# Optimization experiments

Measured on AMD Instinct MI355X. Metric: run time of the kernel, lower is better.

The kernel has to match this reference:

```python
import jax, jax.numpy as jnp
import numpy as np

B, C, H, W = 16, 512, 32, 32
GROUPS = 8
EPS = 1e-5


def setup_inputs() -> dict:
    key = jax.random.key(0)
    ks = jax.random.split(key, 7)
    s = 1.0 / np.sqrt(C)
    return {
        "x": jax.random.normal(ks[0], (B, C, H, W), dtype=jnp.float32),
        "gamma": jnp.ones((C,), dtype=jnp.float32),
        "beta": jnp.zeros((C,), dtype=jnp.float32),
        "w_qkv": jax.random.normal(ks[1], (3 * C, C), dtype=jnp.float32) * s,
        "b_qkv": jnp.zeros((3 * C,), dtype=jnp.float32),
        "w_proj": jax.random.normal(ks[2], (C, C), dtype=jnp.float32) * s,
        "b_proj": jnp.zeros((C,), dtype=jnp.float32),
    }


def group_norm(x, gamma, beta):
    b, c, h, w = x.shape
    xg = x.reshape(b, GROUPS, c // GROUPS, h, w)
    mean = xg.mean(axis=(2, 3, 4), keepdims=True)
    var = xg.var(axis=(2, 3, 4), keepdims=True)
    xn = ((xg - mean) * jax.lax.rsqrt(var + EPS)).reshape(b, c, h, w)
    return xn * gamma[None, :, None, None] + beta[None, :, None, None]


def reference(x, gamma, beta, w_qkv, b_qkv, w_proj, b_proj):
    b, c, h, w = x.shape
    n = h * w
    hn = group_norm(x, gamma, beta)
    # 1x1 conv == channel matmul: [3C, C] x [B, C, N] -> [B, 3C, N]
    qkv = jnp.einsum('oc,bcn->bon', w_qkv, hn.reshape(b, c, n)) + b_qkv[None, :, None]
    q, k, v = jnp.split(qkv, 3, axis=1)  # each [B, C, N]
    scale = c ** (-0.5)
    # scores [B, N, N]: q^T k
    attn = jax.nn.softmax(jnp.einsum('bcn,bcm->bnm', q, k) * scale, axis=-1)
    out = jnp.einsum('bnm,bcm->bcn', attn, v)  # [B, C, N]
    proj = jnp.einsum('oc,bcn->bon', w_proj, out) + b_proj[None, :, None]
    return x + proj.reshape(b, c, h, w)
```

## Files before the change

kernel.cpp:

```cpp
#include <hip/hip_runtime.h>


#define BATCH 16
#define CCH 512
#define NSP 1024
#define EPSV 1e-5f
#define BK 32
#define HT 4096

typedef short bf16x8 __attribute__((ext_vector_type(8)));
typedef float f32x4 __attribute__((ext_vector_type(4)));

__device__ __forceinline__ unsigned short f2bf(float f) {
    unsigned int u = __float_as_uint(f);
    u += 0x7FFF + ((u >> 16) & 1);
    return (unsigned short)(u >> 16);
}

__device__ __forceinline__ void glds16(const void* g, void* l) {
    __builtin_amdgcn_global_load_lds(
        (const __attribute__((address_space(1))) unsigned int*)g,
        (__attribute__((address_space(3))) unsigned int*)l, 16, 0, 0);
}

#define MEMF asm volatile("" ::: "memory")
#define VMW(n) asm volatile("s_waitcnt vmcnt(" #n ")" ::: "memory")

#define XCD_MAP(GX_LOG2, PER, xv, yv, bv)                 \
    const int lin_ = blockIdx.x;                          \
    const int xcd_ = lin_ & 7;                            \
    int slot_ = lin_ >> 3;                                \
    const int hi_ = (slot_ >= (PER)) ? 1 : 0;             \
    const int bv = xcd_ + 8 * hi_;                        \
    slot_ -= hi_ * (PER);                                 \
    const int xv = slot_ & ((1 << (GX_LOG2)) - 1);        \
    const int yv = slot_ >> (GX_LOG2);

__device__ __forceinline__ void gemm128_dbuf(
    const unsigned short* __restrict__ Ag, const unsigned short* __restrict__ Bg,
    int astr, int bstr, int ktot, short* L, f32x4* acc) {
    const int t = threadIdx.x;
    const int w = t >> 6, lane = t & 63;
    const int wr = (w >> 1) * 64, wc = (w & 1) * 64;
    const int fr = lane & 15;
    const int fsw = (((lane >> 4) ^ (fr & 3)) * 8);
    const int r0 = t >> 2;
    const int kc = (((t & 3) ^ (r0 & 3)) * 8);
    const unsigned short* Ap0 = Ag + (size_t)r0 * astr + kc;
    const unsigned short* Ap1 = Ag + (size_t)(r0 + 64) * astr + kc;
    const unsigned short* Bp0 = Bg + (size_t)r0 * bstr + kc;
    const unsigned short* Bp1 = Bg + (size_t)(r0 + 64) * bstr + kc;
    short* lw = L + w * 512;

#define STG(bf, kk) do {                                  \
    short* aw_ = lw + (bf) * (4 * HT);                    \
    short* bw_ = aw_ + 2 * HT;                            \
    glds16(Ap0 + (kk), aw_);                              \
    glds16(Ap1 + (kk), aw_ + 2048);                       \
    glds16(Ap0 + (kk) + 32, aw_ + HT);                    \
    glds16(Ap1 + (kk) + 32, aw_ + HT + 2048);             \
    glds16(Bp0 + (kk), bw_);                              \
    glds16(Bp1 + (kk), bw_ + 2048);                       \
    glds16(Bp0 + (kk) + 32, bw_ + HT);                    \
    glds16(Bp1 + (kk) + 32, bw_ + HT + 2048);             \
  } while (0)

#define CMP(bf) do {                                                        \
    _Pragma("unroll")                                                       \
    for (int h = 0; h < 2; h++) {                                           \
        const short* Ab_ = L + (bf) * (4 * HT) + h * HT;                    \
        const short* Bb_ = Ab_ + 2 * HT;                                    \
        bf16x8 af[4], bfr[4];                                               \
        _Pragma("unroll")                                                   \
        for (int mi = 0; mi < 4; mi++)                                      \
            af[mi] = *(const bf16x8*)(Ab_ + (wr + mi * 16 + fr) * BK + fsw);\
        _Pragma("unroll")                                                   \
        for (int ni = 0; ni < 4; ni++)                                      \
            bfr[ni] = *(const bf16x8*)(Bb_ + (wc + ni * 16 + fr) * BK + fsw);\
        _Pragma("unroll")                                                   \
        for (int mi = 0; mi < 4; mi++)                                      \
            _Pragma("unroll")                                               \
            for (int ni = 0; ni < 4; ni++)                                  \
                acc[mi * 4 + ni] = __builtin_amdgcn_mfma_f32_16x16x32_bf16( \
                    af[mi], bfr[ni], acc[mi * 4 + ni], 0, 0, 0);            \
    } } while (0)

    STG(0, 0);
    for (int k0 = 0; k0 < ktot; k0 += 128) {
        STG(1, k0 + 64);
        VMW(8);
        MEMF; __builtin_amdgcn_s_barrier();
        CMP(0);
        MEMF; __builtin_amdgcn_s_barrier();
        const int kb = (k0 + 128 < ktot) ? k0 + 128 : 0;
        STG(0, kb);
        VMW(8);
        MEMF; __builtin_amdgcn_s_barrier();
        CMP(1);
        MEMF; __builtin_amdgcn_s_barrier();
    }
    VMW(0);
#undef STG
#undef CMP
}

__device__ __forceinline__ void gemm128_sb(
    const unsigned short* __restrict__ Ag, const unsigned short* __restrict__ Bg,
    int astr, int bstr, int ktot, short* Al, short* Bl, f32x4* acc) {
    const int t = threadIdx.x;
    const int w = t >> 6, lane = t & 63;
    const int wr = (w >> 1) * 64, wc = (w & 1) * 64;
    const int fr = lane & 15;
    const int fsw = (((lane >> 4) ^ (fr & 3)) * 8);
    const int r0 = t >> 2;
    const int kc = (((t & 3) ^ (r0 & 3)) * 8);
    const unsigned short* Ap0 = Ag + (size_t)r0 * astr + kc;
    const unsigned short* Ap1 = Ag + (size_t)(r0 + 64) * astr + kc;
    const unsigned short* Bp0 = Bg + (size_t)r0 * bstr + kc;
    const unsigned short* Bp1 = Bg + (size_t)(r0 + 64) * bstr + kc;
    short* Alw = Al + w * 512;
    short* Blw = Bl + w * 512;
    for (int k0 = 0; k0 < ktot; k0 += 64) {
        glds16(Ap0 + k0, Alw);
        glds16(Ap1 + k0, Alw + 2048);
        glds16(Ap0 + k0 + 32, Alw + HT);
        glds16(Ap1 + k0 + 32, Alw + HT + 2048);
        glds16(Bp0 + k0, Blw);
        glds16(Bp1 + k0, Blw + 2048);
        glds16(Bp0 + k0 + 32, Blw + HT);
        glds16(Bp1 + k0 + 32, Blw + HT + 2048);
        __syncthreads();
#pragma unroll
        for (int h = 0; h < 2; h++) {
            const short* Ab = Al + h * HT;
            const short* Bb = Bl + h * HT;
            bf16x8 af[4], bfr[4];
#pragma unroll
            for (int mi = 0; mi < 4; mi++)
                af[mi] = *(const bf16x8*)(Ab + (wr + mi * 16 + fr) * BK + fsw);
#pragma unroll
            for (int ni = 0; ni < 4; ni++)
                bfr[ni] = *(const bf16x8*)(Bb + (wc + ni * 16 + fr) * BK + fsw);
#pragma unroll
            for (int mi = 0; mi < 4; mi++)
#pragma unroll
                for (int ni = 0; ni < 4; ni++)
                    acc[mi * 4 + ni] = __builtin_amdgcn_mfma_f32_16x16x32_bf16(
                        af[mi], bfr[ni], acc[mi * 4 + ni], 0, 0, 0);
        }
        __syncthreads();
    }
}

#define EPI_SETUP()                                          \
    const int t = threadIdx.x, lane = t & 63, w = t >> 6;    \
    const int wr = (w >> 1) * 64, wc = (w & 1) * 64;         \
    const int fr = lane & 15, rr0 = (lane >> 4) * 4;

#define ACC_INIT(acc)                                        \
    f32x4 acc[16];                                           \
    _Pragma("unroll") for (int i = 0; i < 16; i++)           \
        acc[i] = (f32x4){0.f, 0.f, 0.f, 0.f};

__global__ __launch_bounds__(256) void setup_k(
    const float* __restrict__ x, float* __restrict__ stats,
    const float* __restrict__ wa, unsigned short* __restrict__ oa, int na4,
    const float* __restrict__ wb, unsigned short* __restrict__ ob, int nb4,
    float* __restrict__ Lsum, const float* __restrict__ bqv,
    unsigned short* __restrict__ wv_t, float* __restrict__ puv) {
    const int t = threadIdx.x;
    const int bx = blockIdx.x;
    __shared__ float rs[4], rq[4];
    __shared__ __align__(16) unsigned short Tt[64 * 72];
    if (bx < 128) {
        const int bg = bx;
        const float4* xp = (const float4*)(x + (size_t)bg * 65536);
        float s = 0.f, q = 0.f;
#pragma unroll
        for (int i = 0; i < 64; i++) {
            float4 v = xp[t + i * 256];
            s += v.x + v.y + v.z + v.w;
            q += v.x * v.x + v.y * v.y + v.z * v.z + v.w * v.w;
        }
#pragma unroll
        for (int off = 32; off; off >>= 1) {
            s += __shfl_down(s, off);
            q += __shfl_down(q, off);
        }
        const int wave = t >> 6, lane = t & 63;
        if (lane == 0) { rs[wave] = s; rq[wave] = q; }
        __syncthreads();
        if (t == 0) {
            float S = rs[0] + rs[1] + rs[2] + rs[3];
            float Q = rq[0] + rq[1] + rq[2] + rq[3];
            const float inv = 1.f / 65536.f;
            float mean = S * inv;
            float var = Q * inv - mean * mean;
            stats[bg * 2] = mean;
            stats[bg * 2 + 1] = rsqrtf(var + EPSV);
        }
    } else if (bx < 896) {
        int i = (bx - 128) * 256 + t;
        const float* src;
        unsigned short* dst;
        int j;
        if (i < na4) { src = wa; dst = oa; j = i; }
        else { j = i - na4; if (j >= nb4) return; src = wb; dst = ob; }
        float4 v = ((const float4*)src)[j];
        ushort4 o;
        o.x = f2bf(v.x); o.y = f2bf(v.y); o.z = f2bf(v.z); o.w = f2bf(v.w);
        ((ushort4*)dst)[j] = o;
    } else if (bx < 912) {
        int i = (bx - 896) * 256 + t;
        ((float4*)Lsum)[i] = (float4){0.f, 0.f, 0.f, 0.f};
    } else if (bx < 976) {
        const int r = bx - 912;
        const float* src = wa + (size_t)2 * 512 * 512;
        const int to = (r >> 3) * 64, tc = (r & 7) * 64;
        const int ol = t >> 2, cs = t & 3;
#pragma unroll
        for (int j = 0; j < 4; j++) {
            float4 v = *(const float4*)(src + (size_t)(to + ol) * 512 + tc + cs * 16 + j * 4);
            int c = cs * 16 + j * 4;
            Tt[(c + 0) * 72 + ol] = f2bf(v.x);
            Tt[(c + 1) * 72 + ol] = f2bf(v.y);
            Tt[(c + 2) * 72 + ol] = f2bf(v.z);
            Tt[(c + 3) * 72 + ol] = f2bf(v.w);
        }
        __syncthreads();
        const int cl = t >> 2, os = t & 3;
        unsigned short* d = wv_t + (size_t)(tc + cl) * 512 + to + os * 16;
        const unsigned short* s2 = Tt + cl * 72 + os * 16;
        *(uint4*)d = *(const uint4*)s2;
        *(uint4*)(d + 8) = *(const uint4*)(s2 + 8);
    } else {
        const int o = (bx - 976) * 256 + t;
        const float* wr_ = wb + (size_t)o * 512;
        const float* bv = bqv + 1024;
        float s = 0.f;
        for (int vv = 0; vv < 512; vv += 4) {
            s += wr_[vv] * bv[vv] + wr_[vv + 1] * bv[vv + 1]
               + wr_[vv + 2] * bv[vv + 2] + wr_[vv + 3] * bv[vv + 3];
        }
        puv[o] = s;
    }
}

__global__ __launch_bounds__(256) void gn_tr_k(
    const float* __restrict__ x, const float* __restrict__ gamma,
    const float* __restrict__ beta, const float* __restrict__ stats,
    unsigned short* __restrict__ hn_t,
    const unsigned short* __restrict__ wp_bf, const unsigned short* __restrict__ wv_t,
    unsigned short* __restrict__ wpv_bf) {
    __shared__ __align__(16) short SM[4 * HT];
    const int lin = blockIdx.x;
    const int t = threadIdx.x;
    if (lin < 16) {
        const int ot = (lin >> 2) * 128, ct2 = (lin & 3) * 128;
        ACC_INIT(acc);
        gemm128_sb(wp_bf + (size_t)ot * 512, wv_t + (size_t)ct2 * 512,
                   512, 512, 512, SM, SM + 2 * HT, acc);
        EPI_SETUP();
#pragma unroll
        for (int ni = 0; ni < 4; ni++) {
            int col = ct2 + wc + ni * 16 + fr;
#pragma unroll
            for (int mi = 0; mi < 4; mi++) {
                int row = ot + wr + mi * 16 + rr0;
#pragma unroll
                for (int r = 0; r < 4; r++)
                    wpv_bf[(size_t)(row + r) * 512 + col] = f2bf(acc[mi * 4 + ni][r]);
            }
        }
        return;
    }
    const int l2 = lin - 16;
    const int nt = l2 & 15, ct = (l2 >> 4) & 7, b = l2 >> 7;
    unsigned short* T = (unsigned short*)SM;
    const float mean = stats[(b * 8 + ct) * 2];
    const float rstd = stats[(b * 8 + ct) * 2 + 1];
    const int cl = t >> 2, nc = t & 3;
    const int c = ct * 64 + cl;
    const float ga = gamma[c] * rstd;
    const float be = beta[c] - mean * ga;
    const float4* xp = (const float4*)(x + ((size_t)b * CCH + c) * NSP + nt * 64);
#pragma unroll
    for (int j = 0; j < 4; j++) {
        float4 v = xp[nc * 4 + j];
        int n = nc * 16 + j * 4;
        T[(n + 0) * 72 + cl] = f2bf(v.x * ga + be);
        T[(n + 1) * 72 + cl] = f2bf(v.y * ga + be);
        T[(n + 2) * 72 + cl] = f2bf(v.z * ga + be);
        T[(n + 3) * 72 + cl] = f2bf(v.w * ga + be);
    }
    __syncthreads();
    const int nl = t >> 2, cc = t & 3;
    unsigned short* dst = hn_t + ((size_t)b * NSP + nt * 64 + nl) * CCH + ct * 64 + cc * 16;
    const unsigned short* src = T + nl * 72 + cc * 16;
    *(uint4*)dst = *(const uint4*)src;
    *(uint4*)(dst + 8) = *(const uint4*)(src + 8);
}

__global__ __launch_bounds__(256) void gemm_qku_k(
    const unsigned short* __restrict__ hn_t, const unsigned short* __restrict__ wq,
    const float* __restrict__ bq, const unsigned short* __restrict__ wpv_bf,
    const float* __restrict__ puv, unsigned short* __restrict__ QKt,
    unsigned short* __restrict__ Ub) {
    __shared__ __align__(16) short L[8 * HT];
    XCD_MAP(3, 96, xb, y, b);
    const int ntc = xb * 128;
    ACC_INIT(acc);
    if (y < 8) {
        const int mt = y * 128;
        gemm128_dbuf(hn_t + ((size_t)b * NSP + mt) * CCH,
                     wq + (size_t)ntc * CCH, CCH, CCH, CCH, L, acc);
        unsigned short* Ob = QKt + (size_t)b * NSP * 1024;
        EPI_SETUP();
#pragma unroll
        for (int ni = 0; ni < 4; ni++) {
            int col = ntc + wc + ni * 16 + fr;
            float bias = bq[col];
#pragma unroll
            for (int mi = 0; mi < 4; mi++) {
                int row = mt + wr + mi * 16 + rr0;
#pragma unroll
                for (int r = 0; r < 4; r++)
                    Ob[(size_t)(row + r) * 1024 + col] = f2bf(acc[mi * 4 + ni][r] + bias);
            }
        }
    } else {
        const int mt = (y - 8) * 128;
        gemm128_dbuf(wpv_bf + (size_t)mt * 512,
                     hn_t + ((size_t)b * NSP + ntc) * CCH, 512, CCH, 512, L, acc);
        unsigned short* Ob = Ub + (size_t)b * CCH * NSP;
        EPI_SETUP();
#pragma unroll
        for (int mi = 0; mi < 4; mi++) {
            int row = mt + wr + mi * 16 + rr0;
#pragma unroll
            for (int r = 0; r < 4; r++) {
                float bias = puv[row + r];
#pragma unroll
                for (int ni = 0; ni < 4; ni++) {
                    int col = ntc + wc + ni * 16 + fr;
                    Ob[(size_t)(row + r) * NSP + col] = f2bf(acc[mi * 4 + ni][r] + bias);
                }
            }
        }
    }
}

__global__ __launch_bounds__(256) void gemm_scores_k(
    const unsigned short* __restrict__ QKt, unsigned short* __restrict__ expS,
    float* __restrict__ Lsum) {
    __shared__ __align__(16) short L[8 * HT];
    XCD_MAP(3, 64, xb, yb, b);
    const int nt = xb * 128, mt = yb * 128;
    const unsigned short* base = QKt + (size_t)b * NSP * 1024;
    ACC_INIT(acc);
    gemm128_dbuf(base + (size_t)mt * 1024, base + (size_t)nt * 1024 + 512,
                 1024, 1024, 512, L, acc);
    unsigned short* Ob = expS + (size_t)b * NSP * NSP;
    float* Ls = Lsum + (size_t)b * NSP;
    const float scale = 0.044194173824159216f;
    EPI_SETUP();
#pragma unroll
    for (int mi = 0; mi < 4; mi++) {
#pragma unroll
        for (int r = 0; r < 4; r++) {
            const int row = mt + wr + mi * 16 + rr0 + r;
            float rs = 0.f;
#pragma unroll
            for (int ni = 0; ni < 4; ni++) {
                int col = nt + wc + ni * 16 + fr;
                float e = __expf(acc[mi * 4 + ni][r] * scale);
                Ob[(size_t)row * NSP + col] = f2bf(e);
                rs += e;
            }
            rs += __shfl_xor(rs, 1);
            rs += __shfl_xor(rs, 2);
            rs += __shfl_xor(rs, 4);
            rs += __shfl_xor(rs, 8);
            if (fr == 0) atomicAdd(&Ls[row], rs);
        }
    }
}

__global__ __launch_bounds__(256) void gemm_pu_k(
    const unsigned short* __restrict__ Ub, const unsigned short* __restrict__ expS,
    const float* __restrict__ Lsum, const float* __restrict__ x,
    const float* __restrict__ bp, float* __restrict__ out) {
    __shared__ __align__(16) short L[8 * HT];
    XCD_MAP(3, 32, xb, yb, b);
    const int nt = xb * 128, ot = yb * 128;
    ACC_INIT(acc);
    gemm128_dbuf(Ub + ((size_t)b * CCH + ot) * NSP,
                 expS + ((size_t)b * NSP + nt) * NSP, NSP, NSP, NSP, L, acc);
    const float* Ls = Lsum + (size_t)b * NSP;
    const size_t bbase = (size_t)b * CCH * NSP;
    EPI_SETUP();
#pragma unroll
    for (int ni = 0; ni < 4; ni++) {
        int col = nt + wc + ni * 16 + fr;
        float invl = __builtin_amdgcn_rcpf(Ls[col]);
#pragma unroll
        for (int mi = 0; mi < 4; mi++) {
            int row = ot + wr + mi * 16 + rr0;
#pragma unroll
            for (int r = 0; r < 4; r++) {
                size_t idx = bbase + (size_t)(row + r) * NSP + col;
                out[idx] = x[idx] + bp[row + r] + acc[mi * 4 + ni][r] * invl;
            }
        }
    }
}

extern "C" void kernel_launch(void* const* d_in, const int* in_sizes, int n_in,
                              void* d_out, int out_size, void* d_ws, size_t ws_size,
                              hipStream_t stream) {
    const float* x = (const float*)d_in[0];
    const float* gamma = (const float*)d_in[1];
    const float* beta = (const float*)d_in[2];
    const float* w_qkv = (const float*)d_in[3];
    const float* b_qkv = (const float*)d_in[4];
    const float* w_proj = (const float*)d_in[5];
    const float* b_proj = (const float*)d_in[6];
    float* out = (float*)d_out;

    char* ws = (char*)d_ws;
    const size_t MB = 1048576;
    const size_t KB = 1024;
    unsigned short* wqkv_bf = (unsigned short*)ws;
    unsigned short* wproj_bf = (unsigned short*)(ws + 1572864);
    float* stats = (float*)(ws + 2 * MB);
    float* Lsum = (float*)(ws + 2 * MB + 64 * KB);
    float* puv = (float*)(ws + 2 * MB + 128 * KB);
    unsigned short* wv_t = (unsigned short*)(ws + 2 * MB + 256 * KB);
    unsigned short* wpv_bf = (unsigned short*)(ws + 3 * MB);
    unsigned short* hn_t = (unsigned short*)(ws + 4 * MB);
    unsigned short* QKt = (unsigned short*)(ws + 24 * MB);
    unsigned short* Ub = (unsigned short*)(ws + 60 * MB);
    unsigned short* expS = (unsigned short*)(ws + 80 * MB);

    setup_k<<<978, 256, 0, stream>>>(x, stats, w_qkv, wqkv_bf, 131072,
                                     w_proj, wproj_bf, 65536, Lsum, b_qkv,
                                     wv_t, puv);
    gn_tr_k<<<2064, 256, 0, stream>>>(x, gamma, beta, stats, hn_t,
                                      wproj_bf, wv_t, wpv_bf);
    gemm_qku_k<<<1536, 256, 0, stream>>>(hn_t, wqkv_bf, b_qkv, wpv_bf, puv,
                                         QKt, Ub);
    gemm_scores_k<<<1024, 256, 0, stream>>>(QKt, expS, Lsum);
    gemm_pu_k<<<512, 256, 0, stream>>>(Ub, expS, Lsum, x, b_proj, out);
}
```

Measured before the change: 204.6 us.

## Split group-norm statistics over more blocks and revert GEMMs to single-buffered loop

```diff
diff --git a/kernel.cpp b/kernel.cpp
--- a/kernel.cpp
+++ b/kernel.cpp
@@ -36,75 +36,7 @@
     const int xv = slot_ & ((1 << (GX_LOG2)) - 1);        \
     const int yv = slot_ >> (GX_LOG2);
 
-__device__ __forceinline__ void gemm128_dbuf(
-    const unsigned short* __restrict__ Ag, const unsigned short* __restrict__ Bg,
-    int astr, int bstr, int ktot, short* L, f32x4* acc) {
-    const int t = threadIdx.x;
-    const int w = t >> 6, lane = t & 63;
-    const int wr = (w >> 1) * 64, wc = (w & 1) * 64;
-    const int fr = lane & 15;
-    const int fsw = (((lane >> 4) ^ (fr & 3)) * 8);
-    const int r0 = t >> 2;
-    const int kc = (((t & 3) ^ (r0 & 3)) * 8);
-    const unsigned short* Ap0 = Ag + (size_t)r0 * astr + kc;
-    const unsigned short* Ap1 = Ag + (size_t)(r0 + 64) * astr + kc;
-    const unsigned short* Bp0 = Bg + (size_t)r0 * bstr + kc;
-    const unsigned short* Bp1 = Bg + (size_t)(r0 + 64) * bstr + kc;
-    short* lw = L + w * 512;
-
-#define STG(bf, kk) do {                                  \
-    short* aw_ = lw + (bf) * (4 * HT);                    \
-    short* bw_ = aw_ + 2 * HT;                            \
-    glds16(Ap0 + (kk), aw_);                              \
-    glds16(Ap1 + (kk), aw_ + 2048);                       \
-    glds16(Ap0 + (kk) + 32, aw_ + HT);                    \
-    glds16(Ap1 + (kk) + 32, aw_ + HT + 2048);             \
-    glds16(Bp0 + (kk), bw_);                              \
-    glds16(Bp1 + (kk), bw_ + 2048);                       \
-    glds16(Bp0 + (kk) + 32, bw_ + HT);                    \
-    glds16(Bp1 + (kk) + 32, bw_ + HT + 2048);             \
-  } while (0)
-
-#define CMP(bf) do {                                                        \
-    _Pragma("unroll")                                                       \
-    for (int h = 0; h < 2; h++) {                                           \
-        const short* Ab_ = L + (bf) * (4 * HT) + h * HT;                    \
-        const short* Bb_ = Ab_ + 2 * HT;                                    \
-        bf16x8 af[4], bfr[4];                                               \
-        _Pragma("unroll")                                                   \
-        for (int mi = 0; mi < 4; mi++)                                      \
-            af[mi] = *(const bf16x8*)(Ab_ + (wr + mi * 16 + fr) * BK + fsw);\
-        _Pragma("unroll")                                                   \
-        for (int ni = 0; ni < 4; ni++)                                      \
-            bfr[ni] = *(const bf16x8*)(Bb_ + (wc + ni * 16 + fr) * BK + fsw);\
-        _Pragma("unroll")                                                   \
-        for (int mi = 0; mi < 4; mi++)                                      \
-            _Pragma("unroll")                                               \
-            for (int ni = 0; ni < 4; ni++)                                  \
-                acc[mi * 4 + ni] = __builtin_amdgcn_mfma_f32_16x16x32_bf16( \
-                    af[mi], bfr[ni], acc[mi * 4 + ni], 0, 0, 0);            \
-    } } while (0)
-
-    STG(0, 0);
-    for (int k0 = 0; k0 < ktot; k0 += 128) {
-        STG(1, k0 + 64);
-        VMW(8);
-        MEMF; __builtin_amdgcn_s_barrier();
-        CMP(0);
-        MEMF; __builtin_amdgcn_s_barrier();
-        const int kb = (k0 + 128 < ktot) ? k0 + 128 : 0;
-        STG(0, kb);
-        VMW(8);
-        MEMF; __builtin_amdgcn_s_barrier();
-        CMP(1);
-        MEMF; __builtin_amdgcn_s_barrier();
-    }
-    VMW(0);
-#undef STG
-#undef CMP
-}
-
-__device__ __forceinline__ void gemm128_sb(
+__device__ __forceinline__ void gemm128_loop(
     const unsigned short* __restrict__ Ag, const unsigned short* __restrict__ Bg,
     int astr, int bstr, int ktot, short* Al, short* Bl, f32x4* acc) {
     const int t = threadIdx.x;
@@ -152,6 +84,74 @@
     }
 }
 
+__device__ __forceinline__ void gemm128_dbuf(
+    const unsigned short* __restrict__ Ag, const unsigned short* __restrict__ Bg,
+    int astr, int bstr, int ktot, short* L, f32x4* acc) {
+    const int t = threadIdx.x;
+    const int w = t >> 6, lane = t & 63;
+    const int wr = (w >> 1) * 64, wc = (w & 1) * 64;
+    const int fr = lane & 15;
+    const int fsw = (((lane >> 4) ^ (fr & 3)) * 8);
+    const int r0 = t >> 2;
+    const int kc = (((t & 3) ^ (r0 & 3)) * 8);
+    const unsigned short* Ap0 = Ag + (size_t)r0 * astr + kc;
+    const unsigned short* Ap1 = Ag + (size_t)(r0 + 64) * astr + kc;
+    const unsigned short* Bp0 = Bg + (size_t)r0 * bstr + kc;
+    const unsigned short* Bp1 = Bg + (size_t)(r0 + 64) * bstr + kc;
+    short* lw = L + w * 512;
+
+#define STG(bf, kk) do {                                  \
+    short* aw_ = lw + (bf) * (4 * HT);                    \
+    short* bw_ = aw_ + 2 * HT;                            \
+    glds16(Ap0 + (kk), aw_);                              \
+    glds16(Ap1 + (kk), aw_ + 2048);                       \
+    glds16(Ap0 + (kk) + 32, aw_ + HT);                    \
+    glds16(Ap1 + (kk) + 32, aw_ + HT + 2048);             \
+    glds16(Bp0 + (kk), bw_);                              \
+    glds16(Bp1 + (kk), bw_ + 2048);                       \
+    glds16(Bp0 + (kk) + 32, bw_ + HT);                    \
+    glds16(Bp1 + (kk) + 32, bw_ + HT + 2048);             \
+  } while (0)
+
+#define CMP(bf) do {                                                        \
+    _Pragma("unroll")                                                       \
+    for (int h = 0; h < 2; h++) {                                           \
+        const short* Ab_ = L + (bf) * (4 * HT) + h * HT;                    \
+        const short* Bb_ = Ab_ + 2 * HT;                                    \
+        bf16x8 af[4], bfr[4];                                               \
+        _Pragma("unroll")                                                   \
+        for (int mi = 0; mi < 4; mi++)                                      \
+            af[mi] = *(const bf16x8*)(Ab_ + (wr + mi * 16 + fr) * BK + fsw);\
+        _Pragma("unroll")                                                   \
+        for (int ni = 0; ni < 4; ni++)                                      \
+            bfr[ni] = *(const bf16x8*)(Bb_ + (wc + ni * 16 + fr) * BK + fsw);\
+        _Pragma("unroll")                                                   \
+        for (int mi = 0; mi < 4; mi++)                                      \
+            _Pragma("unroll")                                               \
+            for (int ni = 0; ni < 4; ni++)                                  \
+                acc[mi * 4 + ni] = __builtin_amdgcn_mfma_f32_16x16x32_bf16( \
+                    af[mi], bfr[ni], acc[mi * 4 + ni], 0, 0, 0);            \
+    } } while (0)
+
+    STG(0, 0);
+    for (int k0 = 0; k0 < ktot; k0 += 128) {
+        STG(1, k0 + 64);
+        VMW(8);
+        MEMF; __builtin_amdgcn_s_barrier();
+        CMP(0);
+        MEMF; __builtin_amdgcn_s_barrier();
+        const int kb = (k0 + 128 < ktot) ? k0 + 128 : 0;
+        STG(0, kb);
+        VMW(8);
+        MEMF; __builtin_amdgcn_s_barrier();
+        CMP(1);
+        MEMF; __builtin_amdgcn_s_barrier();
+    }
+    VMW(0);
+#undef STG
+#undef CMP
+}
+
 #define EPI_SETUP()                                          \
     const int t = threadIdx.x, lane = t & 63, w = t >> 6;    \
     const int wr = (w >> 1) * 64, wc = (w & 1) * 64;         \
@@ -163,7 +163,7 @@
         acc[i] = (f32x4){0.f, 0.f, 0.f, 0.f};
 
 __global__ __launch_bounds__(256) void setup_k(
-    const float* __restrict__ x, float* __restrict__ stats,
+    const float* __restrict__ x, float* __restrict__ sp,
     const float* __restrict__ wa, unsigned short* __restrict__ oa, int na4,
     const float* __restrict__ wb, unsigned short* __restrict__ ob, int nb4,
     float* __restrict__ Lsum, const float* __restrict__ bqv,
@@ -172,35 +172,30 @@
     const int bx = blockIdx.x;
     __shared__ float rs[4], rq[4];
     __shared__ __align__(16) unsigned short Tt[64 * 72];
-    if (bx < 128) {
-        const int bg = bx;
-        const float4* xp = (const float4*)(x + (size_t)bg * 65536);
-        float s = 0.f, q = 0.f;
-#pragma unroll
-        for (int i = 0; i < 64; i++) {
+    if (bx < 512) {
+        const int bg = bx >> 2, q = bx & 3;
+        const float4* xp = (const float4*)(x + (size_t)bg * 65536 + q * 16384);
+        float s = 0.f, qq = 0.f;
+#pragma unroll
+        for (int i = 0; i < 16; i++) {
             float4 v = xp[t + i * 256];
             s += v.x + v.y + v.z + v.w;
-            q += v.x * v.x + v.y * v.y + v.z * v.z + v.w * v.w;
+            qq += v.x * v.x + v.y * v.y + v.z * v.z + v.w * v.w;
         }
 #pragma unroll
         for (int off = 32; off; off >>= 1) {
             s += __shfl_down(s, off);
-            q += __shfl_down(q, off);
+            qq += __shfl_down(qq, off);
         }
         const int wave = t >> 6, lane = t & 63;
-        if (lane == 0) { rs[wave] = s; rq[wave] = q; }
+        if (lane == 0) { rs[wave] = s; rq[wave] = qq; }
         __syncthreads();
         if (t == 0) {
-            float S = rs[0] + rs[1] + rs[2] + rs[3];
-            float Q = rq[0] + rq[1] + rq[2] + rq[3];
-            const float inv = 1.f / 65536.f;
-            float mean = S * inv;
-            float var = Q * inv - mean * mean;
-            stats[bg * 2] = mean;
-            stats[bg * 2 + 1] = rsqrtf(var + EPSV);
-        }
-    } else if (bx < 896) {
-        int i = (bx - 128) * 256 + t;
+            sp[bx * 2] = rs[0] + rs[1] + rs[2] + rs[3];
+            sp[bx * 2 + 1] = rq[0] + rq[1] + rq[2] + rq[3];
+        }
+    } else if (bx < 1280) {
+        int i = (bx - 512) * 256 + t;
         const float* src;
         unsigned short* dst;
         int j;
@@ -210,11 +205,11 @@
         ushort4 o;
         o.x = f2bf(v.x); o.y = f2bf(v.y); o.z = f2bf(v.z); o.w = f2bf(v.w);
         ((ushort4*)dst)[j] = o;
-    } else if (bx < 912) {
-        int i = (bx - 896) * 256 + t;
+    } else if (bx < 1296) {
+        int i = (bx - 1280) * 256 + t;
         ((float4*)Lsum)[i] = (float4){0.f, 0.f, 0.f, 0.f};
-    } else if (bx < 976) {
-        const int r = bx - 912;
+    } else if (bx < 1360) {
+        const int r = bx - 1296;
         const float* src = wa + (size_t)2 * 512 * 512;
         const int to = (r >> 3) * 64, tc = (r & 7) * 64;
         const int ol = t >> 2, cs = t & 3;
@@ -234,7 +229,7 @@
         *(uint4*)d = *(const uint4*)s2;
         *(uint4*)(d + 8) = *(const uint4*)(s2 + 8);
     } else {
-        const int o = (bx - 976) * 256 + t;
+        const int o = (bx - 1360) * 256 + t;
         const float* wr_ = wb + (size_t)o * 512;
         const float* bv = bqv + 1024;
         float s = 0.f;
@@ -248,7 +243,7 @@
 
 __global__ __launch_bounds__(256) void gn_tr_k(
     const float* __restrict__ x, const float* __restrict__ gamma,
-    const float* __restrict__ beta, const float* __restrict__ stats,
+    const float* __restrict__ beta, const float* __restrict__ sp,
     unsigned short* __restrict__ hn_t,
     const unsigned short* __restrict__ wp_bf, const unsigned short* __restrict__ wv_t,
     unsigned short* __restrict__ wpv_bf) {
@@ -258,8 +253,8 @@
     if (lin < 16) {
         const int ot = (lin >> 2) * 128, ct2 = (lin & 3) * 128;
         ACC_INIT(acc);
-        gemm128_sb(wp_bf + (size_t)ot * 512, wv_t + (size_t)ct2 * 512,
-                   512, 512, 512, SM, SM + 2 * HT, acc);
+        gemm128_loop(wp_bf + (size_t)ot * 512, wv_t + (size_t)ct2 * 512,
+                     512, 512, 512, SM, SM + 2 * HT, acc);
         EPI_SETUP();
 #pragma unroll
         for (int ni = 0; ni < 4; ni++) {
@@ -277,8 +272,16 @@
     const int l2 = lin - 16;
     const int nt = l2 & 15, ct = (l2 >> 4) & 7, b = l2 >> 7;
     unsigned short* T = (unsigned short*)SM;
-    const float mean = stats[(b * 8 + ct) * 2];
-    const float rstd = stats[(b * 8 + ct) * 2 + 1];
+    const int bg = b * 8 + ct;
+    float S = 0.f, Q = 0.f;
+#pragma unroll
+    for (int qq = 0; qq < 4; qq++) {
+        S += sp[(bg * 4 + qq) * 2];
+        Q += sp[(bg * 4 + qq) * 2 + 1];
+    }
+    const float inv = 1.f / 65536.f;
+    const float mean = S * inv;
+    const float rstd = rsqrtf(Q * inv - mean * mean + EPSV);
     const int cl = t >> 2, nc = t & 3;
     const int c = ct * 64 + cl;
     const float ga = gamma[c] * rstd;
@@ -306,14 +309,14 @@
     const float* __restrict__ bq, const unsigned short* __restrict__ wpv_bf,
     const float* __restrict__ puv, unsigned short* __restrict__ QKt,
     unsigned short* __restrict__ Ub) {
-    __shared__ __align__(16) short L[8 * HT];
+    __shared__ __align__(16) short Al[2 * HT], Bl[2 * HT];
     XCD_MAP(3, 96, xb, y, b);
     const int ntc = xb * 128;
     ACC_INIT(acc);
     if (y < 8) {
         const int mt = y * 128;
-        gemm128_dbuf(hn_t + ((size_t)b * NSP + mt) * CCH,
-                     wq + (size_t)ntc * CCH, CCH, CCH, CCH, L, acc);
+        gemm128_loop(hn_t + ((size_t)b * NSP + mt) * CCH,
+                     wq + (size_t)ntc * CCH, CCH, CCH, CCH, Al, Bl, acc);
         unsigned short* Ob = QKt + (size_t)b * NSP * 1024;
         EPI_SETUP();
 #pragma unroll
@@ -330,8 +333,8 @@
         }
     } else {
         const int mt = (y - 8) * 128;
-        gemm128_dbuf(wpv_bf + (size_t)mt * 512,
-                     hn_t + ((size_t)b * NSP + ntc) * CCH, 512, CCH, 512, L, acc);
+        gemm128_loop(wpv_bf + (size_t)mt * 512,
+                     hn_t + ((size_t)b * NSP + ntc) * CCH, 512, CCH, 512, Al, Bl, acc);
         unsigned short* Ob = Ub + (size_t)b * CCH * NSP;
         EPI_SETUP();
 #pragma unroll
@@ -353,13 +356,13 @@
 __global__ __launch_bounds__(256) void gemm_scores_k(
     const unsigned short* __restrict__ QKt, unsigned short* __restrict__ expS,
     float* __restrict__ Lsum) {
-    __shared__ __align__(16) short L[8 * HT];
+    __shared__ __align__(16) short Al[2 * HT], Bl[2 * HT];
     XCD_MAP(3, 64, xb, yb, b);
     const int nt = xb * 128, mt = yb * 128;
     const unsigned short* base = QKt + (size_t)b * NSP * 1024;
     ACC_INIT(acc);
-    gemm128_dbuf(base + (size_t)mt * 1024, base + (size_t)nt * 1024 + 512,
-                 1024, 1024, 512, L, acc);
+    gemm128_loop(base + (size_t)mt * 1024, base + (size_t)nt * 1024 + 512,
+                 1024, 1024, 512, Al, Bl, acc);
     unsigned short* Ob = expS + (size_t)b * NSP * NSP;
     float* Ls = Lsum + (size_t)b * NSP;
     const float scale = 0.044194173824159216f;
@@ -432,7 +435,7 @@
     const size_t KB = 1024;
     unsigned short* wqkv_bf = (unsigned short*)ws;
     unsigned short* wproj_bf = (unsigned short*)(ws + 1572864);
-    float* stats = (float*)(ws + 2 * MB);
+    float* sp = (float*)(ws + 2 * MB);
     float* Lsum = (float*)(ws + 2 * MB + 64 * KB);
     float* puv = (float*)(ws + 2 * MB + 128 * KB);
     unsigned short* wv_t = (unsigned short*)(ws + 2 * MB + 256 * KB);
@@ -442,10 +445,10 @@
     unsigned short* Ub = (unsigned short*)(ws + 60 * MB);
     unsigned short* expS = (unsigned short*)(ws + 80 * MB);
 
-    setup_k<<<978, 256, 0, stream>>>(x, stats, w_qkv, wqkv_bf, 131072,
-                                     w_proj, wproj_bf, 65536, Lsum, b_qkv,
-                                     wv_t, puv);
-    gn_tr_k<<<2064, 256, 0, stream>>>(x, gamma, beta, stats, hn_t,
+    setup_k<<<1362, 256, 0, stream>>>(x, sp, w_qkv, wqkv_bf, 131072,
+                                      w_proj, wproj_bf, 65536, Lsum, b_qkv,
+                                      wv_t, puv);
+    gn_tr_k<<<2064, 256, 0, stream>>>(x, gamma, beta, sp, hn_t,
                                       wproj_bf, wv_t, wpv_bf);
     gemm_qku_k<<<1536, 256, 0, stream>>>(hn_t, wqkv_bf, b_qkv, wpv_bf, puv,
                                          QKt, Ub);
```

Result: slower. 212.1 us (+3.7%).

## Use 8-wave 512-thread blocks for the 128x128 bf16 GEMM kernels

Applied to the files above, without the earlier changes.

```diff
diff --git a/kernel.cpp b/kernel.cpp
--- a/kernel.cpp
+++ b/kernel.cpp
@@ -36,65 +36,58 @@
     const int xv = slot_ & ((1 << (GX_LOG2)) - 1);        \
     const int yv = slot_ >> (GX_LOG2);
 
-__device__ __forceinline__ void gemm128_dbuf(
+__device__ __forceinline__ void gemm128_dbuf8(
     const unsigned short* __restrict__ Ag, const unsigned short* __restrict__ Bg,
     int astr, int bstr, int ktot, short* L, f32x4* acc) {
     const int t = threadIdx.x;
     const int w = t >> 6, lane = t & 63;
-    const int wr = (w >> 1) * 64, wc = (w & 1) * 64;
+    const int wr = (w >> 2) * 64, wc = (w & 3) * 32;
     const int fr = lane & 15;
     const int fsw = (((lane >> 4) ^ (fr & 3)) * 8);
     const int r0 = t >> 2;
     const int kc = (((t & 3) ^ (r0 & 3)) * 8);
     const unsigned short* Ap0 = Ag + (size_t)r0 * astr + kc;
-    const unsigned short* Ap1 = Ag + (size_t)(r0 + 64) * astr + kc;
     const unsigned short* Bp0 = Bg + (size_t)r0 * bstr + kc;
-    const unsigned short* Bp1 = Bg + (size_t)(r0 + 64) * bstr + kc;
     short* lw = L + w * 512;
 
 #define STG(bf, kk) do {                                  \
-    short* aw_ = lw + (bf) * (4 * HT);                    \
-    short* bw_ = aw_ + 2 * HT;                            \
-    glds16(Ap0 + (kk), aw_);                              \
-    glds16(Ap1 + (kk), aw_ + 2048);                       \
-    glds16(Ap0 + (kk) + 32, aw_ + HT);                    \
-    glds16(Ap1 + (kk) + 32, aw_ + HT + 2048);             \
-    glds16(Bp0 + (kk), bw_);                              \
-    glds16(Bp1 + (kk), bw_ + 2048);                       \
-    glds16(Bp0 + (kk) + 32, bw_ + HT);                    \
-    glds16(Bp1 + (kk) + 32, bw_ + HT + 2048);             \
+    short* p_ = lw + (bf) * (4 * HT);                     \
+    glds16(Ap0 + (kk), p_);                               \
+    glds16(Ap0 + (kk) + 32, p_ + HT);                     \
+    glds16(Bp0 + (kk), p_ + 2 * HT);                      \
+    glds16(Bp0 + (kk) + 32, p_ + 3 * HT);                 \
   } while (0)
 
 #define CMP(bf) do {                                                        \
     _Pragma("unroll")                                                       \
     for (int h = 0; h < 2; h++) {                                           \
         const short* Ab_ = L + (bf) * (4 * HT) + h * HT;                    \
-        const short* Bb_ = Ab_ + 2 * HT;                                    \
-        bf16x8 af[4], bfr[4];                                               \
+        const short* Bb_ = L + (bf) * (4 * HT) + (2 + h) * HT;              \
+        bf16x8 af[4], bfr[2];                                               \
         _Pragma("unroll")                                                   \
         for (int mi = 0; mi < 4; mi++)                                      \
             af[mi] = *(const bf16x8*)(Ab_ + (wr + mi * 16 + fr) * BK + fsw);\
         _Pragma("unroll")                                                   \
-        for (int ni = 0; ni < 4; ni++)                                      \
+        for (int ni = 0; ni < 2; ni++)                                      \
             bfr[ni] = *(const bf16x8*)(Bb_ + (wc + ni * 16 + fr) * BK + fsw);\
         _Pragma("unroll")                                                   \
         for (int mi = 0; mi < 4; mi++)                                      \
             _Pragma("unroll")                                               \
-            for (int ni = 0; ni < 4; ni++)                                  \
-                acc[mi * 4 + ni] = __builtin_amdgcn_mfma_f32_16x16x32_bf16( \
-                    af[mi], bfr[ni], acc[mi * 4 + ni], 0, 0, 0);            \
+            for (int ni = 0; ni < 2; ni++)                                  \
+                acc[mi * 2 + ni] = __builtin_amdgcn_mfma_f32_16x16x32_bf16( \
+                    af[mi], bfr[ni], acc[mi * 2 + ni], 0, 0, 0);            \
     } } while (0)
 
     STG(0, 0);
     for (int k0 = 0; k0 < ktot; k0 += 128) {
         STG(1, k0 + 64);
-        VMW(8);
+        VMW(4);
         MEMF; __builtin_amdgcn_s_barrier();
         CMP(0);
         MEMF; __builtin_amdgcn_s_barrier();
         const int kb = (k0 + 128 < ktot) ? k0 + 128 : 0;
         STG(0, kb);
-        VMW(8);
+        VMW(4);
         MEMF; __builtin_amdgcn_s_barrier();
         CMP(1);
         MEMF; __builtin_amdgcn_s_barrier();
@@ -157,9 +150,19 @@
     const int wr = (w >> 1) * 64, wc = (w & 1) * 64;         \
     const int fr = lane & 15, rr0 = (lane >> 4) * 4;
 
+#define EPI8()                                               \
+    const int t = threadIdx.x, lane = t & 63, w8 = t >> 6;   \
+    const int wr = (w8 >> 2) * 64, wc = (w8 & 3) * 32;       \
+    const int fr = lane & 15, rr0 = (lane >> 4) * 4;
+
 #define ACC_INIT(acc)                                        \
     f32x4 acc[16];                                           \
     _Pragma("unroll") for (int i = 0; i < 16; i++)           \
+        acc[i] = (f32x4){0.f, 0.f, 0.f, 0.f};
+
+#define ACC_INIT8(acc)                                       \
+    f32x4 acc[8];                                            \
+    _Pragma("unroll") for (int i = 0; i < 8; i++)            \
         acc[i] = (f32x4){0.f, 0.f, 0.f, 0.f};
 
 __global__ __launch_bounds__(256) void setup_k(
@@ -301,7 +304,7 @@
     *(uint4*)(dst + 8) = *(const uint4*)(src + 8);
 }
 
-__global__ __launch_bounds__(256) void gemm_qku_k(
+__global__ __launch_bounds__(512) void gemm_qku_k(
     const unsigned short* __restrict__ hn_t, const unsigned short* __restrict__ wq,
     const float* __restrict__ bq, const unsigned short* __restrict__ wpv_bf,
     const float* __restrict__ puv, unsigned short* __restrict__ QKt,
@@ -309,15 +312,15 @@
     __shared__ __align__(16) short L[8 * HT];
     XCD_MAP(3, 96, xb, y, b);
     const int ntc = xb * 128;
-    ACC_INIT(acc);
+    ACC_INIT8(acc);
     if (y < 8) {
         const int mt = y * 128;
-        gemm128_dbuf(hn_t + ((size_t)b * NSP + mt) * CCH,
-                     wq + (size_t)ntc * CCH, CCH, CCH, CCH, L, acc);
+        gemm128_dbuf8(hn_t + ((size_t)b * NSP + mt) * CCH,
+                      wq + (size_t)ntc * CCH, CCH, CCH, CCH, L, acc);
         unsigned short* Ob = QKt + (size_t)b * NSP * 1024;
-        EPI_SETUP();
-#pragma unroll
-        for (int ni = 0; ni < 4; ni++) {
+        EPI8();
+#pragma unroll
+        for (int ni = 0; ni < 2; ni++) {
             int col = ntc + wc + ni * 16 + fr;
             float bias = bq[col];
 #pragma unroll
@@ -325,15 +328,15 @@
                 int row = mt + wr + mi * 16 + rr0;
 #pragma unroll
                 for (int r = 0; r < 4; r++)
-                    Ob[(size_t)(row + r) * 1024 + col] = f2bf(acc[mi * 4 + ni][r] + bias);
+                    Ob[(size_t)(row + r) * 1024 + col] = f2bf(acc[mi * 2 + ni][r] + bias);
             }
         }
     } else {
         const int mt = (y - 8) * 128;
-        gemm128_dbuf(wpv_bf + (size_t)mt * 512,
-                     hn_t + ((size_t)b * NSP + ntc) * CCH, 512, CCH, 512, L, acc);
+        gemm128_dbuf8(wpv_bf + (size_t)mt * 512,
+                      hn_t + ((size_t)b * NSP + ntc) * CCH, 512, CCH, 512, L, acc);
         unsigned short* Ob = Ub + (size_t)b * CCH * NSP;
-        EPI_SETUP();
+        EPI8();
 #pragma unroll
         for (int mi = 0; mi < 4; mi++) {
             int row = mt + wr + mi * 16 + rr0;
@@ -341,29 +344,29 @@
             for (int r = 0; r < 4; r++) {
                 float bias = puv[row + r];
 #pragma unroll
-                for (int ni = 0; ni < 4; ni++) {
+                for (int ni = 0; ni < 2; ni++) {
                     int col = ntc + wc + ni * 16 + fr;
-                    Ob[(size_t)(row + r) * NSP + col] = f2bf(acc[mi * 4 + ni][r] + bias);
+                    Ob[(size_t)(row + r) * NSP + col] = f2bf(acc[mi * 2 + ni][r] + bias);
                 }
             }
         }
     }
 }
 
-__global__ __launch_bounds__(256) void gemm_scores_k(
+__global__ __launch_bounds__(512) void gemm_scores_k(
     const unsigned short* __restrict__ QKt, unsigned short* __restrict__ expS,
     float* __restrict__ Lsum) {
     __shared__ __align__(16) short L[8 * HT];
     XCD_MAP(3, 64, xb, yb, b);
     const int nt = xb * 128, mt = yb * 128;
     const unsigned short* base = QKt + (size_t)b * NSP * 1024;
-    ACC_INIT(acc);
-    gemm128_dbuf(base + (size_t)mt * 1024, base + (size_t)nt * 1024 + 512,
-                 1024, 1024, 512, L, acc);
+    ACC_INIT8(acc);
+    gemm128_dbuf8(base + (size_t)mt * 1024, base + (size_t)nt * 1024 + 512,
+                  1024, 1024, 512, L, acc);
     unsigned short* Ob = expS + (size_t)b * NSP * NSP;
     float* Ls = Lsum + (size_t)b * NSP;
     const float scale = 0.044194173824159216f;
-    EPI_SETUP();
+    EPI8();
 #pragma unroll
     for (int mi = 0; mi < 4; mi++) {
 #pragma unroll
@@ -371,9 +374,9 @@
             const int row = mt + wr + mi * 16 + rr0 + r;
             float rs = 0.f;
 #pragma unroll
-            for (int ni = 0; ni < 4; ni++) {
+            for (int ni = 0; ni < 2; ni++) {
                 int col = nt + wc + ni * 16 + fr;
-                float e = __expf(acc[mi * 4 + ni][r] * scale);
+                float e = __expf(acc[mi * 2 + ni][r] * scale);
                 Ob[(size_t)row * NSP + col] = f2bf(e);
                 rs += e;
             }
@@ -386,21 +389,21 @@
     }
 }
 
-__global__ __launch_bounds__(256) void gemm_pu_k(
+__global__ __launch_bounds__(512) void gemm_pu_k(
     const unsigned short* __restrict__ Ub, const unsigned short* __restrict__ expS,
     const float* __restrict__ Lsum, const float* __restrict__ x,
     const float* __restrict__ bp, float* __restrict__ out) {
     __shared__ __align__(16) short L[8 * HT];
     XCD_MAP(3, 32, xb, yb, b);
     const int nt = xb * 128, ot = yb * 128;
-    ACC_INIT(acc);
-    gemm128_dbuf(Ub + ((size_t)b * CCH + ot) * NSP,
-                 expS + ((size_t)b * NSP + nt) * NSP, NSP, NSP, NSP, L, acc);
+    ACC_INIT8(acc);
+    gemm128_dbuf8(Ub + ((size_t)b * CCH + ot) * NSP,
+                  expS + ((size_t)b * NSP + nt) * NSP, NSP, NSP, NSP, L, acc);
     const float* Ls = Lsum + (size_t)b * NSP;
     const size_t bbase = (size_t)b * CCH * NSP;
-    EPI_SETUP();
-#pragma unroll
-    for (int ni = 0; ni < 4; ni++) {
+    EPI8();
+#pragma unroll
+    for (int ni = 0; ni < 2; ni++) {
         int col = nt + wc + ni * 16 + fr;
         float invl = __builtin_amdgcn_rcpf(Ls[col]);
 #pragma unroll
@@ -409,7 +412,7 @@
 #pragma unroll
             for (int r = 0; r < 4; r++) {
                 size_t idx = bbase + (size_t)(row + r) * NSP + col;
-                out[idx] = x[idx] + bp[row + r] + acc[mi * 4 + ni][r] * invl;
+                out[idx] = x[idx] + bp[row + r] + acc[mi * 2 + ni][r] * invl;
             }
         }
     }
@@ -447,8 +450,8 @@
                                      wv_t, puv);
     gn_tr_k<<<2064, 256, 0, stream>>>(x, gamma, beta, stats, hn_t,
                                       wproj_bf, wv_t, wpv_bf);
-    gemm_qku_k<<<1536, 256, 0, stream>>>(hn_t, wqkv_bf, b_qkv, wpv_bf, puv,
+    gemm_qku_k<<<1536, 512, 0, stream>>>(hn_t, wqkv_bf, b_qkv, wpv_bf, puv,
                                          QKt, Ub);
-    gemm_scores_k<<<1024, 256, 0, stream>>>(QKt, expS, Lsum);
-    gemm_pu_k<<<512, 256, 0, stream>>>(Ub, expS, Lsum, x, b_proj, out);
-}
+    gemm_scores_k<<<1024, 512, 0, stream>>>(QKt, expS, Lsum);
+    gemm_pu_k<<<512, 512, 0, stream>>>(Ub, expS, Lsum, x, b_proj, out);
+}
```

New measurement: 208.0 us. No clear change (+1.7%).
